# Optimization experiments

Hardware: AMD Instinct MI355X
Metric: run time of the kernel (lower is better)

The kernel has to match this reference:

```python
import jax, jax.numpy as jnp
import numpy as np

E = 32      # particle_embed_dim = q/k/v head out dim
G = 2       # nof_net_types (conv groups)
NEG_SLOPE = 0.01


def _glin(x, w, b, groups):
    """Grouped 1x1 conv on (M, C, 1, 1) == grouped linear.
    x: (M, Cin), w: (Cout, Cin//groups), b: (Cout,)."""
    M = x.shape[0]
    Cout = w.shape[0]
    xg = x.reshape(M, groups, -1)                 # (M, G, Cin/G)
    wg = w.reshape(groups, Cout // groups, -1)    # (G, Cout/G, Cin/G)
    y = jnp.einsum('mgi,goi->mgo', xg, wg).reshape(M, Cout)
    return y + b


def setup_inputs() -> dict:
    key = jax.random.key(0)
    ks = jax.random.split(key, 9)
    B, N = 32, 1024
    s = 0.05
    return {
        'x_e':   jax.random.normal(ks[0], (B, N, G * E), dtype=jnp.float32),
        'w_qkv': jax.random.normal(ks[1], (3 * G * E, E), dtype=jnp.float32) * s,
        'b_qkv': jax.random.normal(ks[2], (3 * G * E,), dtype=jnp.float32) * s,
        'w_h1':  jax.random.normal(ks[3], (G * E, 2 * E), dtype=jnp.float32) * s,
        'b_h1':  jax.random.normal(ks[4], (G * E,), dtype=jnp.float32) * s,
        'w_h10': jax.random.normal(ks[5], (G * E, E), dtype=jnp.float32) * s,
        'b_h10': jax.random.normal(ks[6], (G * E,), dtype=jnp.float32) * s,
        'w_h11': jax.random.normal(ks[7], (G * E, E), dtype=jnp.float32) * s,
        'b_h11': jax.random.normal(ks[8], (G * E,), dtype=jnp.float32) * s,
    }


def reference(x_e, w_qkv, b_qkv, w_h1, b_h1, w_h10, b_h10, w_h11, b_h11):
    B, N, D = x_e.shape                      # D = G*E = 64
    act = lambda z: jnp.where(z >= 0, z, NEG_SLOPE * z)

    # grouped 1x1-conv QKV projection
    qkv = _glin(x_e.reshape(B * N, D), w_qkv, b_qkv, G)        # (B*N, 3*G*E)
    qkv = qkv.reshape(B, N, G, 3, E).transpose(0, 2, 3, 1, 4)  # (B, G, 3, N, E)
    q, k, v = qkv[:, :, 0], qkv[:, :, 1], qkv[:, :, 2]         # each (B, G, N, E)

    # NOTE: module divides k by sqrt(E) and logits by sqrt(E) again -> 1/E total
    scale = 1.0 / E
    ip = jnp.einsum('bgne,bgme->bgnm', q, k) * scale           # (B, G, N, N)
    sip = jax.nn.softmax(ip, axis=-1)
    attn = jnp.einsum('bgnm,bgme->bgne', sip, v)               # (B, G, N, E)

    # concat pre-attention v with attention output, regroup per-particle
    x_xe = jnp.concatenate([v, attn], axis=3)                  # (B, G, N, 2E)
    x_xe = x_xe.transpose(0, 2, 1, 3).reshape(B * N, G * 2 * E)  # (B*N, 128)

    h = act(_glin(x_xe, w_h1, b_h1, G))
    h = act(_glin(h, w_h10, b_h10, G))
    h = act(_glin(h, w_h11, b_h11, G))
    return h.reshape(B * N, G * E, 1, 1)
```

## Files before the change

### kernel.cpp

```cpp
#include <hip/hip_runtime.h>

#define B_ 32
#define N_ 1024
#define NEG 0.01f
#define QSC (1.4426950408889634f/32.0f)

using half8  = __attribute__((ext_vector_type(8))) _Float16;
using half4  = __attribute__((ext_vector_type(4))) _Float16;
using half2  = __attribute__((ext_vector_type(2))) _Float16;
using fp16x2 = __attribute__((ext_vector_type(2))) __fp16;
using floatx4 = __attribute__((ext_vector_type(4))) float;

#if defined(__has_builtin)
#if __has_builtin(__builtin_amdgcn_exp2f)
#define EXP2(x) __builtin_amdgcn_exp2f(x)
#endif
#endif
#ifndef EXP2
#define EXP2(x) exp2f(x)
#endif

#define MFMA32 __builtin_amdgcn_mfma_f32_16x16x32_f16
#define MFMA16 __builtin_amdgcn_mfma_f32_16x16x16f16

__device__ inline half2 pkcvt(float a, float b) {
    fp16x2 r = __builtin_amdgcn_cvt_pkrtz(a, b);
    return __builtin_bit_cast(half2, r);
}

__device__ inline half8 cvt8(float4 a, float4 b) {
    half2 p0 = pkcvt(a.x, a.y);
    half2 p1 = pkcvt(a.z, a.w);
    half2 p2 = pkcvt(b.x, b.y);
    half2 p3 = pkcvt(b.z, b.w);
    half8 h = { p0[0],p0[1], p1[0],p1[1], p2[0],p2[1], p3[0],p3[1] };
    return h;
}

struct __align__(16) Smem {
    _Float16 wsh[96*36];
    float    bsh[96];
    _Float16 Kst[2][128*40];
    _Float16 Vtst[2][32*136];
    union {
        _Float16 qs[128*40];
        _Float16 xs[128*72];
    } u;
    float bl1[32], bl10[32], bl11[32];
};

__global__ __launch_bounds__(256, 2) void fused_kernel(
    const float* __restrict__ x, const float* __restrict__ w_qkv, const float* __restrict__ b_qkv,
    const float* __restrict__ w_h1,  const float* __restrict__ b_h1,
    const float* __restrict__ w_h10, const float* __restrict__ b_h10,
    const float* __restrict__ w_h11, const float* __restrict__ b_h11,
    float* __restrict__ out)
{
    __shared__ Smem sm;
    int t = threadIdx.x;
    int bid = blockIdx.x;
    int xcd = bid & 7, j = bid >> 3;
    int bg = xcd*8 + (j >> 3);
    int qtile = j & 7;
    int b = bg >> 1, g = bg & 1;
    int qbase = qtile * 128;
    int lane = t & 63, w = t >> 6;
    int L15 = lane & 15, quad = lane >> 4;

    for (int idx = t; idx < 96*32; idx += 256) {
        int r = idx >> 5, c = idx & 31;
        float wv = w_qkv[(g*96 + r)*32 + c];
        sm.wsh[r*36 + c] = (_Float16)(r < 32 ? wv*QSC : wv);
    }
    if (t < 96) sm.bsh[t] = b_qkv[g*96 + t];
    if (t < 32) {
        sm.bl1[t]  = b_h1[g*32+t];
        sm.bl10[t] = b_h10[g*32+t];
        sm.bl11[t] = b_h11[g*32+t];
    }
    __syncthreads();

    half8 bwq[2], bwk[2], bwv[2];
    floatx4 cq[2], ck[2], cv[2];
    #pragma unroll
    for (int et = 0; et < 2; et++) {
        bwq[et] = *(const half8*)&sm.wsh[(     et*16 + L15)*36 + quad*8];
        bwk[et] = *(const half8*)&sm.wsh[(32 + et*16 + L15)*36 + quad*8];
        bwv[et] = *(const half8*)&sm.wsh[(64 + et*16 + L15)*36 + quad*8];
        float bq = sm.bsh[     et*16 + L15] * QSC;
        float bk = sm.bsh[32 + et*16 + L15];
        float bv = sm.bsh[64 + et*16 + L15];
        cq[et] = (floatx4){bq,bq,bq,bq};
        ck[et] = (floatx4){bk,bk,bk,bk};
        cv[et] = (floatx4){bv,bv,bv,bv};
    }

    {
        floatx4 dq[2][2];
        #pragma unroll
        for (int mt = 0; mt < 2; mt++) {
            const float* p = x + ((size_t)b*N_ + qbase + w*32 + mt*16 + L15)*64 + g*32 + quad*8;
            half8 axq = cvt8(*(const float4*)p, *(const float4*)(p + 4));
            dq[mt][0] = MFMA32(axq, bwq[0], cq[0], 0,0,0);
            dq[mt][1] = MFMA32(axq, bwq[1], cq[1], 0,0,0);
        }
        #pragma unroll
        for (int mt = 0; mt < 2; mt++)
            #pragma unroll
            for (int et = 0; et < 2; et++)
                #pragma unroll
                for (int r = 0; r < 4; r++)
                    sm.u.qs[(w*32 + mt*16 + quad*4 + r)*40 + et*16 + L15] =
                        (_Float16)dq[mt][et][r];
    }
    __syncthreads();
    half8 bq0 = *(const half8*)&sm.u.qs[(w*32 +      L15)*40 + quad*8];
    half8 bq1 = *(const half8*)&sm.u.qs[(w*32 + 16 + L15)*40 + quad*8];
    __syncthreads();

    float4 xf0[2], xf1[2];
    auto prefetch = [&](int tile) {
        #pragma unroll
        for (int mt = 0; mt < 2; mt++) {
            const float* p = x + ((size_t)b*N_ + tile*128 + w*32 + mt*16 + L15)*64 + g*32 + quad*8;
            xf0[mt] = *(const float4*)p;
            xf1[mt] = *(const float4*)(p + 4);
        }
    };
    auto proj_tile = [&](int tile, int buf) {
        floatx4 dK[2][2], dV[2][2];
        #pragma unroll
        for (int mt = 0; mt < 2; mt++) {
            half8 axk = cvt8(xf0[mt], xf1[mt]);
            dK[mt][0] = MFMA32(axk, bwk[0], ck[0], 0,0,0);
            dK[mt][1] = MFMA32(axk, bwk[1], ck[1], 0,0,0);
            dV[mt][0] = MFMA32(axk, bwv[0], cv[0], 0,0,0);
            dV[mt][1] = MFMA32(axk, bwv[1], cv[1], 0,0,0);
        }
        #pragma unroll
        for (int mt = 0; mt < 2; mt++) {
            int rb = w*32 + mt*16 + quad*4;
            #pragma unroll
            for (int et = 0; et < 2; et++) {
                half2 k01 = pkcvt(dK[mt][et][0], dK[mt][et][1]);
                half2 k23 = pkcvt(dK[mt][et][2], dK[mt][et][3]);
                half2 v01 = pkcvt(dV[mt][et][0], dV[mt][et][1]);
                half2 v23 = pkcvt(dV[mt][et][2], dV[mt][et][3]);
                half4 vh = { v01[0], v01[1], v23[0], v23[1] };
                sm.Kst[buf][(rb+0)*40 + et*16 + L15] = k01[0];
                sm.Kst[buf][(rb+1)*40 + et*16 + L15] = k01[1];
                sm.Kst[buf][(rb+2)*40 + et*16 + L15] = k23[0];
                sm.Kst[buf][(rb+3)*40 + et*16 + L15] = k23[1];
                *(half4*)&sm.Vtst[buf][(et*16 + L15)*136 + rb] = vh;
                if (tile == qtile) {
                    #pragma unroll
                    for (int r = 0; r < 4; r++)
                        sm.u.xs[(rb + r)*72 + et*16 + L15] = vh[r];
                }
            }
        }
    };

    prefetch(0);
    proj_tile(0, 0);
    __syncthreads();

    floatx4 o00 = {0.f,0.f,0.f,0.f}, o01 = o00, o10 = o00, o11 = o00;
    float lsum0 = 0.f, lsum1 = 0.f;

    for (int kt = 0; kt < 8; kt++) {
        int cur = kt & 1;
        if (kt < 7) prefetch(kt + 1);
        __builtin_amdgcn_s_setprio(1);
        #pragma unroll
        for (int mt8 = 0; mt8 < 8; mt8++) {
            half8 ak = *(const half8*)&sm.Kst[cur][(mt8*16 + L15)*40 + quad*8];
            floatx4 zz = {0.f,0.f,0.f,0.f};
            floatx4 s0 = MFMA32(ak, bq0, zz, 0,0,0);
            floatx4 s1 = MFMA32(ak, bq1, zz, 0,0,0);
            float p00 = EXP2(s0.x), p01 = EXP2(s0.y), p02 = EXP2(s0.z), p03 = EXP2(s0.w);
            float p10 = EXP2(s1.x), p11 = EXP2(s1.y), p12 = EXP2(s1.z), p13 = EXP2(s1.w);
            lsum0 += (p00+p01)+(p02+p03);
            lsum1 += (p10+p11)+(p12+p13);
            half2 pa = pkcvt(p00, p01);
            half2 pb = pkcvt(p02, p03);
            half2 pc = pkcvt(p10, p11);
            half2 pd = pkcvt(p12, p13);
            half4 a0 = { pa[0], pa[1], pb[0], pb[1] };
            half4 a1 = { pc[0], pc[1], pd[0], pd[1] };
            half4 bv0 = *(const half4*)&sm.Vtst[cur][      L15*136 + mt8*16 + quad*4];
            half4 bv1 = *(const half4*)&sm.Vtst[cur][(16 + L15)*136 + mt8*16 + quad*4];
            o00 = MFMA16(a0, bv0, o00, 0,0,0);
            o01 = MFMA16(a0, bv1, o01, 0,0,0);
            o10 = MFMA16(a1, bv0, o10, 0,0,0);
            o11 = MFMA16(a1, bv1, o11, 0,0,0);
        }
        __builtin_amdgcn_s_setprio(0);
        if (kt < 7) {
            proj_tile(kt + 1, 1 - cur);
            __syncthreads();
        }
    }

    lsum0 += __shfl_xor(lsum0, 16, 64); lsum0 += __shfl_xor(lsum0, 32, 64);
    lsum1 += __shfl_xor(lsum1, 16, 64); lsum1 += __shfl_xor(lsum1, 32, 64);
    float inv0 = 1.0f / lsum0;
    float inv1 = 1.0f / lsum1;
    float li[2][4];
    #pragma unroll
    for (int r = 0; r < 4; r++) {
        li[0][r] = __shfl(inv0, quad*4 + r, 64);
        li[1][r] = __shfl(inv1, quad*4 + r, 64);
    }

    {
        const floatx4* ofr[2][2] = { {&o00,&o01}, {&o10,&o11} };
        #pragma unroll
        for (int nt = 0; nt < 2; nt++) {
            #pragma unroll
            for (int et = 0; et < 2; et++) {
                floatx4 ov = *ofr[nt][et];
                sm.u.xs[(w*32+nt*16+quad*4+0)*72 + 32 + et*16 + L15] = (_Float16)(ov[0]*li[nt][0]);
                sm.u.xs[(w*32+nt*16+quad*4+1)*72 + 32 + et*16 + L15] = (_Float16)(ov[1]*li[nt][1]);
                sm.u.xs[(w*32+nt*16+quad*4+2)*72 + 32 + et*16 + L15] = (_Float16)(ov[2]*li[nt][2]);
                sm.u.xs[(w*32+nt*16+quad*4+3)*72 + 32 + et*16 + L15] = (_Float16)(ov[3]*li[nt][3]);
            }
        }
    }

    half4 a1f[2][4], a2f[2][2], a3f[2][2];
    #pragma unroll
    for (int mt = 0; mt < 2; mt++) {
        #pragma unroll
        for (int kt = 0; kt < 4; kt++) {
            float4 f = *(const float4*)(w_h1 + (size_t)(g*32+mt*16+L15)*64 + kt*16 + quad*4);
            half2 ha = pkcvt(f.x, f.y);
            half2 hb = pkcvt(f.z, f.w);
            half4 h = { ha[0], ha[1], hb[0], hb[1] };
            a1f[mt][kt] = h;
        }
        #pragma unroll
        for (int kt = 0; kt < 2; kt++) {
            float4 f = *(const float4*)(w_h10 + (size_t)(g*32+mt*16+L15)*32 + kt*16 + quad*4);
            half2 ha = pkcvt(f.x, f.y);
            half2 hb = pkcvt(f.z, f.w);
            half4 h = { ha[0], ha[1], hb[0], hb[1] };
            a2f[mt][kt] = h;
            float4 f2 = *(const float4*)(w_h11 + (size_t)(g*32+mt*16+L15)*32 + kt*16 + quad*4);
            half2 hc = pkcvt(f2.x, f2.y);
            half2 hd = pkcvt(f2.z, f2.w);
            half4 h2 = { hc[0], hc[1], hd[0], hd[1] };
            a3f[mt][kt] = h2;
        }
    }

    floatx4 d1[2][2];
    #pragma unroll
    for (int mt = 0; mt < 2; mt++) {
        float4 bb = *(const float4*)&sm.bl1[mt*16 + quad*4];
        floatx4 seed = { bb.x, bb.y, bb.z, bb.w };
        d1[mt][0] = seed; d1[mt][1] = seed;
    }
    #pragma unroll
    for (int nt = 0; nt < 2; nt++)
        #pragma unroll
        for (int kt = 0; kt < 4; kt++) {
            half4 b1 = *(const half4*)&sm.u.xs[(w*32+nt*16+L15)*72 + kt*16 + quad*4];
            d1[0][nt] = MFMA16(a1f[0][kt], b1, d1[0][nt], 0,0,0);
            d1[1][nt] = MFMA16(a1f[1][kt], b1, d1[1][nt], 0,0,0);
        }
    half4 h1b[2][2];
    #pragma unroll
    for (int mt = 0; mt < 2; mt++)
        #pragma unroll
        for (int nt = 0; nt < 2; nt++) {
            float v0 = d1[mt][nt][0]; v0 = (v0>=0.f)?v0:NEG*v0;
            float v1 = d1[mt][nt][1]; v1 = (v1>=0.f)?v1:NEG*v1;
            float v2 = d1[mt][nt][2]; v2 = (v2>=0.f)?v2:NEG*v2;
            float v3 = d1[mt][nt][3]; v3 = (v3>=0.f)?v3:NEG*v3;
            half2 ha = pkcvt(v0, v1);
            half2 hb = pkcvt(v2, v3);
            half4 h = { ha[0], ha[1], hb[0], hb[1] };
            h1b[mt][nt] = h;
        }
    floatx4 d2[2][2];
    #pragma unroll
    for (int mt = 0; mt < 2; mt++) {
        float4 bb = *(const float4*)&sm.bl10[mt*16 + quad*4];
        floatx4 seed = { bb.x, bb.y, bb.z, bb.w };
        d2[mt][0] = seed; d2[mt][1] = seed;
    }
    #pragma unroll
    for (int mt = 0; mt < 2; mt++)
        #pragma unroll
        for (int nt = 0; nt < 2; nt++)
            #pragma unroll
            for (int kt = 0; kt < 2; kt++)
                d2[mt][nt] = MFMA16(a2f[mt][kt], h1b[kt][nt], d2[mt][nt], 0,0,0);
    half4 h2b[2][2];
    #pragma unroll
    for (int mt = 0; mt < 2; mt++)
        #pragma unroll
        for (int nt = 0; nt < 2; nt++) {
            float v0 = d2[mt][nt][0]; v0 = (v0>=0.f)?v0:NEG*v0;
            float v1 = d2[mt][nt][1]; v1 = (v1>=0.f)?v1:NEG*v1;
            float v2 = d2[mt][nt][2]; v2 = (v2>=0.f)?v2:NEG*v2;
            float v3 = d2[mt][nt][3]; v3 = (v3>=0.f)?v3:NEG*v3;
            half2 ha = pkcvt(v0, v1);
            half2 hb = pkcvt(v2, v3);
            half4 h = { ha[0], ha[1], hb[0], hb[1] };
            h2b[mt][nt] = h;
        }
    floatx4 d3[2][2];
    #pragma unroll
    for (int mt = 0; mt < 2; mt++) {
        float4 bb = *(const float4*)&sm.bl11[mt*16 + quad*4];
        floatx4 seed = { bb.x, bb.y, bb.z, bb.w };
        d3[mt][0] = seed; d3[mt][1] = seed;
    }
    #pragma unroll
    for (int mt = 0; mt < 2; mt++)
        #pragma unroll
        for (int nt = 0; nt < 2; nt++)
            #pragma unroll
            for (int kt = 0; kt < 2; kt++)
                d3[mt][nt] = MFMA16(a3f[mt][kt], h2b[kt][nt], d3[mt][nt], 0,0,0);
    #pragma unroll
    for (int mt = 0; mt < 2; mt++)
        #pragma unroll
        for (int nt = 0; nt < 2; nt++) {
            float4 ov;
            ov.x = d3[mt][nt][0]; ov.x = (ov.x>=0.f)?ov.x:NEG*ov.x;
            ov.y = d3[mt][nt][1]; ov.y = (ov.y>=0.f)?ov.y:NEG*ov.y;
            ov.z = d3[mt][nt][2]; ov.z = (ov.z>=0.f)?ov.z:NEG*ov.z;
            ov.w = d3[mt][nt][3]; ov.w = (ov.w>=0.f)?ov.w:NEG*ov.w;
            *(float4*)(out + ((size_t)b*N_ + qbase + w*32 + nt*16 + L15)*64 + g*32 + mt*16 + quad*4) = ov;
        }
}

extern "C" void kernel_launch(void* const* d_in, const int* in_sizes, int n_in,
                              void* d_out, int out_size, void* d_ws, size_t ws_size,
                              hipStream_t stream) {
    const float* x_e   = (const float*)d_in[0];
    const float* w_qkv = (const float*)d_in[1];
    const float* b_qkv = (const float*)d_in[2];
    const float* w_h1  = (const float*)d_in[3];
    const float* b_h1  = (const float*)d_in[4];
    const float* w_h10 = (const float*)d_in[5];
    const float* b_h10 = (const float*)d_in[6];
    const float* w_h11 = (const float*)d_in[7];
    const float* b_h11 = (const float*)d_in[8];
    float* out = (float*)d_out;

    hipLaunchKernelGGL(fused_kernel, dim3(B_*2*8), dim3(256), 0, stream,
                       x_e, w_qkv, b_qkv, w_h1, b_h1, w_h10, b_h10, w_h11, b_h11, out);
}
```

Measured before the change: 97.86 us.

## Share per-tile K/V projections across blocks via global workspace and flags

New measurement: 274.5 us. +180.5%, slower.

```diff
diff --git a/kernel.cpp b/kernel.cpp
--- a/kernel.cpp
+++ b/kernel.cpp
@@ -4,6 +4,7 @@
 #define N_ 1024
 #define NEG 0.01f
 #define QSC (1.4426950408889634f/32.0f)
+#define MAGIC 0x5EEDBEA7u
 
 using half8  = __attribute__((ext_vector_type(8))) _Float16;
 using half4  = __attribute__((ext_vector_type(4))) _Float16;
@@ -37,13 +38,18 @@
     return h;
 }
 
+__device__ __forceinline__ void gload16(const _Float16* g, _Float16* l) {
+    __builtin_amdgcn_global_load_lds(
+        (const __attribute__((address_space(1))) unsigned int*)g,
+        (__attribute__((address_space(3))) unsigned int*)l, 16, 0, 0);
+}
+
 struct __align__(16) Smem {
     _Float16 wsh[96*36];
     float    bsh[96];
-    _Float16 Kst[2][128*40];
-    _Float16 Vtst[2][32*136];
     union {
-        _Float16 qs[128*40];
+        struct { _Float16 qs[128*40]; _Float16 kst[128*32]; _Float16 vt[32*136]; } p1;
+        struct { _Float16 K[2][4096]; _Float16 Vt[2][4096]; } p2;
         _Float16 xs[128*72];
     } u;
     float bl1[32], bl10[32], bl11[32];
@@ -54,7 +60,8 @@
     const float* __restrict__ w_h1,  const float* __restrict__ b_h1,
     const float* __restrict__ w_h10, const float* __restrict__ b_h10,
     const float* __restrict__ w_h11, const float* __restrict__ b_h11,
-    float* __restrict__ out)
+    float* __restrict__ out, _Float16* __restrict__ Kg, _Float16* __restrict__ Vtg,
+    unsigned* __restrict__ flags)
 {
     __shared__ Smem sm;
     int t = threadIdx.x;
@@ -66,6 +73,7 @@
     int qbase = qtile * 128;
     int lane = t & 63, w = t >> 6;
     int L15 = lane & 15, quad = lane >> 4;
+    const floatx4 zz = {0.f,0.f,0.f,0.f};
 
     for (int idx = t; idx < 96*32; idx += 256) {
         int r = idx >> 5, c = idx & 31;
@@ -81,101 +89,114 @@
     __syncthreads();
 
     half8 bwq[2], bwk[2], bwv[2];
-    floatx4 cq[2], ck[2], cv[2];
+    float bqv[2], bvv[2];
     #pragma unroll
     for (int et = 0; et < 2; et++) {
         bwq[et] = *(const half8*)&sm.wsh[(     et*16 + L15)*36 + quad*8];
         bwk[et] = *(const half8*)&sm.wsh[(32 + et*16 + L15)*36 + quad*8];
         bwv[et] = *(const half8*)&sm.wsh[(64 + et*16 + L15)*36 + quad*8];
-        float bq = sm.bsh[     et*16 + L15] * QSC;
-        float bk = sm.bsh[32 + et*16 + L15];
-        float bv = sm.bsh[64 + et*16 + L15];
-        cq[et] = (floatx4){bq,bq,bq,bq};
-        ck[et] = (floatx4){bk,bk,bk,bk};
-        cv[et] = (floatx4){bv,bv,bv,bv};
-    }
+        bqv[et] = sm.bsh[     et*16 + L15] * QSC;
+        bvv[et] = sm.bsh[64 + et*16 + L15];
+    }
+
+    half4 vown[2][2];
+    #pragma unroll
+    for (int mt = 0; mt < 2; mt++) {
+        const float* p = x + ((size_t)b*N_ + qbase + w*32 + mt*16 + L15)*64 + g*32 + quad*8;
+        half8 ax = cvt8(*(const float4*)p, *(const float4*)(p + 4));
+        int rb = w*32 + mt*16 + quad*4;
+        #pragma unroll
+        for (int et = 0; et < 2; et++) {
+            floatx4 cq = {bqv[et],bqv[et],bqv[et],bqv[et]};
+            floatx4 cv = {bvv[et],bvv[et],bvv[et],bvv[et]};
+            floatx4 dq = MFMA32(ax, bwq[et], cq, 0,0,0);
+            floatx4 dk = MFMA32(ax, bwk[et], zz, 0,0,0);
+            floatx4 dv = MFMA32(ax, bwv[et], cv, 0,0,0);
+            #pragma unroll
+            for (int r = 0; r < 4; r++)
+                sm.u.p1.qs[(rb+r)*40 + et*16 + L15] = (_Float16)dq[r];
+            half2 k01 = pkcvt(dk[0], dk[1]);
+            half2 k23 = pkcvt(dk[2], dk[3]);
+            sm.u.p1.kst[(rb+0)*32 + et*16 + L15] = k01[0];
+            sm.u.p1.kst[(rb+1)*32 + et*16 + L15] = k01[1];
+            sm.u.p1.kst[(rb+2)*32 + et*16 + L15] = k23[0];
+            sm.u.p1.kst[(rb+3)*32 + et*16 + L15] = k23[1];
+            half2 v01 = pkcvt(dv[0], dv[1]);
+            half2 v23 = pkcvt(dv[2], dv[3]);
+            half4 vh = { v01[0], v01[1], v23[0], v23[1] };
+            *(half4*)&sm.u.p1.vt[(et*16 + L15)*136 + rb] = vh;
+            vown[mt][et] = vh;
+        }
+    }
+    __syncthreads();
+
+    half8 bq0 = *(const half8*)&sm.u.p1.qs[(w*32 +      L15)*40 + quad*8];
+    half8 bq1 = *(const half8*)&sm.u.p1.qs[(w*32 + 16 + L15)*40 + quad*8];
 
     {
-        floatx4 dq[2][2];
-        #pragma unroll
-        for (int mt = 0; mt < 2; mt++) {
-            const float* p = x + ((size_t)b*N_ + qbase + w*32 + mt*16 + L15)*64 + g*32 + quad*8;
-            half8 axq = cvt8(*(const float4*)p, *(const float4*)(p + 4));
-            dq[mt][0] = MFMA32(axq, bwq[0], cq[0], 0,0,0);
-            dq[mt][1] = MFMA32(axq, bwq[1], cq[1], 0,0,0);
-        }
-        #pragma unroll
-        for (int mt = 0; mt < 2; mt++)
-            #pragma unroll
-            for (int et = 0; et < 2; et++)
-                #pragma unroll
-                for (int r = 0; r < 4; r++)
-                    sm.u.qs[(w*32 + mt*16 + quad*4 + r)*40 + et*16 + L15] =
-                        (_Float16)dq[mt][et][r];
-    }
+        const float4* s4 = (const float4*)sm.u.p1.kst;
+        float4* d4 = (float4*)(Kg + (size_t)bg*32768 + (size_t)qbase*32);
+        d4[t] = s4[t];
+        d4[t+256] = s4[t+256];
+    }
+    {
+        int e = t >> 3, c = t & 7;
+        const float4* s4 = (const float4*)&sm.u.p1.vt[e*136 + c*16];
+        float4* d4 = (float4*)(Vtg + (size_t)bg*32768 + (size_t)e*1024 + qbase + c*16);
+        d4[0] = s4[0];
+        d4[1] = s4[1];
+    }
+
+    __threadfence();
     __syncthreads();
-    half8 bq0 = *(const half8*)&sm.u.qs[(w*32 +      L15)*40 + quad*8];
-    half8 bq1 = *(const half8*)&sm.u.qs[(w*32 + 16 + L15)*40 + quad*8];
+    if (t == 0)
+        __hip_atomic_store(&flags[bg*8 + qtile], MAGIC,
+                           __ATOMIC_RELEASE, __HIP_MEMORY_SCOPE_AGENT);
+
+    const _Float16* kgB = Kg  + (size_t)bg*32768;
+    const _Float16* vgB = Vtg + (size_t)bg*32768;
+    const unsigned* fB = &flags[bg*8];
+    auto wait_tile = [&](int tj) {
+        for (int s_ = 0; s_ < (1<<20); ++s_) {
+            if (__hip_atomic_load(&fB[tj], __ATOMIC_ACQUIRE,
+                                  __HIP_MEMORY_SCOPE_AGENT) == MAGIC)
+                break;
+        }
+    };
+    int kRow   = lane >> 2;
+    int kChunk = (lane & 3) ^ ((lane >> 3) & 3);
+
+    auto stage = [&](int tile, int bufi) {
+        #pragma unroll
+        for (int d = 0; d < 2; d++) {
+            gload16(kgB + (size_t)(tile*128 + w*32 + d*16 + kRow)*32 + kChunk*8,
+                    &sm.u.p2.K[bufi][w*1024 + d*512]);
+            int e  = w*8 + d*4 + (lane >> 4);
+            int vc = (lane & 15) ^ (e & 7);
+            gload16(vgB + (size_t)e*1024 + tile*128 + vc*8,
+                    &sm.u.p2.Vt[bufi][w*1024 + d*512]);
+        }
+    };
+
+    floatx4 o00 = zz, o01 = zz, o10 = zz, o11 = zz;
+    float lsum0 = 0.f, lsum1 = 0.f;
+    int kswz = (quad ^ ((L15 >> 1) & 3)) * 8;
+    int vswz = ((L15 & 7) << 1);
+
+    wait_tile(0);
+    stage(0, 0);
     __syncthreads();
-
-    float4 xf0[2], xf1[2];
-    auto prefetch = [&](int tile) {
-        #pragma unroll
-        for (int mt = 0; mt < 2; mt++) {
-            const float* p = x + ((size_t)b*N_ + tile*128 + w*32 + mt*16 + L15)*64 + g*32 + quad*8;
-            xf0[mt] = *(const float4*)p;
-            xf1[mt] = *(const float4*)(p + 4);
-        }
-    };
-    auto proj_tile = [&](int tile, int buf) {
-        floatx4 dK[2][2], dV[2][2];
-        #pragma unroll
-        for (int mt = 0; mt < 2; mt++) {
-            half8 axk = cvt8(xf0[mt], xf1[mt]);
-            dK[mt][0] = MFMA32(axk, bwk[0], ck[0], 0,0,0);
-            dK[mt][1] = MFMA32(axk, bwk[1], ck[1], 0,0,0);
-            dV[mt][0] = MFMA32(axk, bwv[0], cv[0], 0,0,0);
-            dV[mt][1] = MFMA32(axk, bwv[1], cv[1], 0,0,0);
-        }
-        #pragma unroll
-        for (int mt = 0; mt < 2; mt++) {
-            int rb = w*32 + mt*16 + quad*4;
-            #pragma unroll
-            for (int et = 0; et < 2; et++) {
-                half2 k01 = pkcvt(dK[mt][et][0], dK[mt][et][1]);
-                half2 k23 = pkcvt(dK[mt][et][2], dK[mt][et][3]);
-                half2 v01 = pkcvt(dV[mt][et][0], dV[mt][et][1]);
-                half2 v23 = pkcvt(dV[mt][et][2], dV[mt][et][3]);
-                half4 vh = { v01[0], v01[1], v23[0], v23[1] };
-                sm.Kst[buf][(rb+0)*40 + et*16 + L15] = k01[0];
-                sm.Kst[buf][(rb+1)*40 + et*16 + L15] = k01[1];
-                sm.Kst[buf][(rb+2)*40 + et*16 + L15] = k23[0];
-                sm.Kst[buf][(rb+3)*40 + et*16 + L15] = k23[1];
-                *(half4*)&sm.Vtst[buf][(et*16 + L15)*136 + rb] = vh;
-                if (tile == qtile) {
-                    #pragma unroll
-                    for (int r = 0; r < 4; r++)
-                        sm.u.xs[(rb + r)*72 + et*16 + L15] = vh[r];
-                }
-            }
-        }
-    };
-
-    prefetch(0);
-    proj_tile(0, 0);
-    __syncthreads();
-
-    floatx4 o00 = {0.f,0.f,0.f,0.f}, o01 = o00, o10 = o00, o11 = o00;
-    float lsum0 = 0.f, lsum1 = 0.f;
 
     for (int kt = 0; kt < 8; kt++) {
         int cur = kt & 1;
-        if (kt < 7) prefetch(kt + 1);
+        if (kt < 7) {
+            wait_tile(kt + 1);
+            stage(kt + 1, cur ^ 1);
+        }
         __builtin_amdgcn_s_setprio(1);
         #pragma unroll
-        for (int mt8 = 0; mt8 < 8; mt8++) {
-            half8 ak = *(const half8*)&sm.Kst[cur][(mt8*16 + L15)*40 + quad*8];
-            floatx4 zz = {0.f,0.f,0.f,0.f};
+        for (int m8 = 0; m8 < 8; m8++) {
+            half8 ak = *(const half8*)&sm.u.p2.K[cur][(m8*16 + L15)*32 + kswz];
             floatx4 s0 = MFMA32(ak, bq0, zz, 0,0,0);
             floatx4 s1 = MFMA32(ak, bq1, zz, 0,0,0);
             float p00 = EXP2(s0.x), p01 = EXP2(s0.y), p02 = EXP2(s0.z), p03 = EXP2(s0.w);
@@ -188,18 +209,16 @@
             half2 pd = pkcvt(p12, p13);
             half4 a0 = { pa[0], pa[1], pb[0], pb[1] };
             half4 a1 = { pc[0], pc[1], pd[0], pd[1] };
-            half4 bv0 = *(const half4*)&sm.Vtst[cur][      L15*136 + mt8*16 + quad*4];
-            half4 bv1 = *(const half4*)&sm.Vtst[cur][(16 + L15)*136 + mt8*16 + quad*4];
+            int vg_ = ((m8*4 + quad) ^ vswz) * 4;
+            half4 bv0 = *(const half4*)&sm.u.p2.Vt[cur][      L15*128 + vg_];
+            half4 bv1 = *(const half4*)&sm.u.p2.Vt[cur][(16 + L15)*128 + vg_];
             o00 = MFMA16(a0, bv0, o00, 0,0,0);
             o01 = MFMA16(a0, bv1, o01, 0,0,0);
             o10 = MFMA16(a1, bv0, o10, 0,0,0);
             o11 = MFMA16(a1, bv1, o11, 0,0,0);
         }
         __builtin_amdgcn_s_setprio(0);
-        if (kt < 7) {
-            proj_tile(kt + 1, 1 - cur);
-            __syncthreads();
-        }
+        __syncthreads();
     }
 
     lsum0 += __shfl_xor(lsum0, 16, 64); lsum0 += __shfl_xor(lsum0, 32, 64);
@@ -217,13 +236,17 @@
         const floatx4* ofr[2][2] = { {&o00,&o01}, {&o10,&o11} };
         #pragma unroll
         for (int nt = 0; nt < 2; nt++) {
+            int rb = w*32 + nt*16 + quad*4;
             #pragma unroll
             for (int et = 0; et < 2; et++) {
+                #pragma unroll
+                for (int r = 0; r < 4; r++)
+                    sm.u.xs[(rb+r)*72 + et*16 + L15] = vown[nt][et][r];
                 floatx4 ov = *ofr[nt][et];
-                sm.u.xs[(w*32+nt*16+quad*4+0)*72 + 32 + et*16 + L15] = (_Float16)(ov[0]*li[nt][0]);
-                sm.u.xs[(w*32+nt*16+quad*4+1)*72 + 32 + et*16 + L15] = (_Float16)(ov[1]*li[nt][1]);
-                sm.u.xs[(w*32+nt*16+quad*4+2)*72 + 32 + et*16 + L15] = (_Float16)(ov[2]*li[nt][2]);
-                sm.u.xs[(w*32+nt*16+quad*4+3)*72 + 32 + et*16 + L15] = (_Float16)(ov[3]*li[nt][3]);
+                sm.u.xs[(rb+0)*72 + 32 + et*16 + L15] = (_Float16)(ov[0]*li[nt][0]);
+                sm.u.xs[(rb+1)*72 + 32 + et*16 + L15] = (_Float16)(ov[1]*li[nt][1]);
+                sm.u.xs[(rb+2)*72 + 32 + et*16 + L15] = (_Float16)(ov[2]*li[nt][2]);
+                sm.u.xs[(rb+3)*72 + 32 + et*16 + L15] = (_Float16)(ov[3]*li[nt][3]);
             }
         }
     }
@@ -352,6 +375,11 @@
     const float* b_h11 = (const float*)d_in[8];
     float* out = (float*)d_out;
 
-    hipLaunchKernelGGL(fused_kernel, dim3(B_*2*8), dim3(256), 0, stream,
-                       x_e, w_qkv, b_qkv, w_h1, b_h1, w_h10, b_h10, w_h11, b_h11, out);
-}
+    _Float16* Kg   = (_Float16*)d_ws;
+    _Float16* Vtg  = (_Float16*)d_ws + (1u<<21);
+    unsigned* flags = (unsigned*)((_Float16*)d_ws + (2u<<21));
+
+    hipLaunchKernelGGL(fused_kernel, dim3(512), dim3(256), 0, stream,
+                       x_e, w_qkv, b_qkv, w_h1, b_h1, w_h10, b_h10, w_h11, b_h11,
+                       out, Kg, Vtg, flags);
+}
```

## Shrink shared memory and registers to raise occupancy to three blocks per CU

Applied to the files above, without the earlier changes.

Result: slower. 111.1 us (+13.5%).

```diff
diff --git a/kernel.cpp b/kernel.cpp
--- a/kernel.cpp
+++ b/kernel.cpp
@@ -40,16 +40,17 @@
 struct __align__(16) Smem {
     _Float16 wsh[96*36];
     float    bsh[96];
-    _Float16 Kst[2][128*40];
-    _Float16 Vtst[2][32*136];
     union {
-        _Float16 qs[128*40];
+        struct {
+            _Float16 Kst[2][128*36];
+            _Float16 Vtst[2][32*136];
+        } a;
         _Float16 xs[128*72];
     } u;
     float bl1[32], bl10[32], bl11[32];
 };
 
-__global__ __launch_bounds__(256, 2) void fused_kernel(
+__global__ __launch_bounds__(256, 3) void fused_kernel(
     const float* __restrict__ x, const float* __restrict__ w_qkv, const float* __restrict__ b_qkv,
     const float* __restrict__ w_h1,  const float* __restrict__ b_h1,
     const float* __restrict__ w_h10, const float* __restrict__ b_h10,
@@ -66,6 +67,7 @@
     int qbase = qtile * 128;
     int lane = t & 63, w = t >> 6;
     int L15 = lane & 15, quad = lane >> 4;
+    const floatx4 zz = {0.f,0.f,0.f,0.f};
 
     for (int idx = t; idx < 96*32; idx += 256) {
         int r = idx >> 5, c = idx & 31;
@@ -81,43 +83,37 @@
     __syncthreads();
 
     half8 bwq[2], bwk[2], bwv[2];
-    floatx4 cq[2], ck[2], cv[2];
+    floatx4 cv[2];
     #pragma unroll
     for (int et = 0; et < 2; et++) {
         bwq[et] = *(const half8*)&sm.wsh[(     et*16 + L15)*36 + quad*8];
         bwk[et] = *(const half8*)&sm.wsh[(32 + et*16 + L15)*36 + quad*8];
         bwv[et] = *(const half8*)&sm.wsh[(64 + et*16 + L15)*36 + quad*8];
-        float bq = sm.bsh[     et*16 + L15] * QSC;
-        float bk = sm.bsh[32 + et*16 + L15];
         float bv = sm.bsh[64 + et*16 + L15];
-        cq[et] = (floatx4){bq,bq,bq,bq};
-        ck[et] = (floatx4){bk,bk,bk,bk};
         cv[et] = (floatx4){bv,bv,bv,bv};
     }
 
-    {
-        floatx4 dq[2][2];
-        #pragma unroll
-        for (int mt = 0; mt < 2; mt++) {
-            const float* p = x + ((size_t)b*N_ + qbase + w*32 + mt*16 + L15)*64 + g*32 + quad*8;
-            half8 axq = cvt8(*(const float4*)p, *(const float4*)(p + 4));
-            dq[mt][0] = MFMA32(axq, bwq[0], cq[0], 0,0,0);
-            dq[mt][1] = MFMA32(axq, bwq[1], cq[1], 0,0,0);
-        }
-        #pragma unroll
-        for (int mt = 0; mt < 2; mt++)
-            #pragma unroll
-            for (int et = 0; et < 2; et++)
-                #pragma unroll
-                for (int r = 0; r < 4; r++)
-                    sm.u.qs[(w*32 + mt*16 + quad*4 + r)*40 + et*16 + L15] =
-                        (_Float16)dq[mt][et][r];
+    _Float16* qs = sm.u.a.Kst[1];
+
+    #pragma unroll
+    for (int mt = 0; mt < 2; mt++) {
+        const float* p = x + ((size_t)b*N_ + qbase + w*32 + mt*16 + L15)*64 + g*32 + quad*8;
+        half8 axq = cvt8(*(const float4*)p, *(const float4*)(p + 4));
+        #pragma unroll
+        for (int et = 0; et < 2; et++) {
+            float bq = sm.bsh[et*16 + L15] * QSC;
+            floatx4 cq = {bq,bq,bq,bq};
+            floatx4 dq = MFMA32(axq, bwq[et], cq, 0,0,0);
+            #pragma unroll
+            for (int r = 0; r < 4; r++)
+                qs[(w*32 + mt*16 + quad*4 + r)*36 + et*16 + L15] = (_Float16)dq[r];
+        }
     }
     __syncthreads();
-    half8 bq0 = *(const half8*)&sm.u.qs[(w*32 +      L15)*40 + quad*8];
-    half8 bq1 = *(const half8*)&sm.u.qs[(w*32 + 16 + L15)*40 + quad*8];
-    __syncthreads();
-
+    half8 bq0 = *(const half8*)&qs[(w*32 +      L15)*36 + quad*8];
+    half8 bq1 = *(const half8*)&qs[(w*32 + 16 + L15)*36 + quad*8];
+
+    half4 vown[2][2];
     float4 xf0[2], xf1[2];
     auto prefetch = [&](int tile) {
         #pragma unroll
@@ -132,8 +128,8 @@
         #pragma unroll
         for (int mt = 0; mt < 2; mt++) {
             half8 axk = cvt8(xf0[mt], xf1[mt]);
-            dK[mt][0] = MFMA32(axk, bwk[0], ck[0], 0,0,0);
-            dK[mt][1] = MFMA32(axk, bwk[1], ck[1], 0,0,0);
+            dK[mt][0] = MFMA32(axk, bwk[0], zz, 0,0,0);
+            dK[mt][1] = MFMA32(axk, bwk[1], zz, 0,0,0);
             dV[mt][0] = MFMA32(axk, bwv[0], cv[0], 0,0,0);
             dV[mt][1] = MFMA32(axk, bwv[1], cv[1], 0,0,0);
         }
@@ -147,16 +143,12 @@
                 half2 v01 = pkcvt(dV[mt][et][0], dV[mt][et][1]);
                 half2 v23 = pkcvt(dV[mt][et][2], dV[mt][et][3]);
                 half4 vh = { v01[0], v01[1], v23[0], v23[1] };
-                sm.Kst[buf][(rb+0)*40 + et*16 + L15] = k01[0];
-                sm.Kst[buf][(rb+1)*40 + et*16 + L15] = k01[1];
-                sm.Kst[buf][(rb+2)*40 + et*16 + L15] = k23[0];
-                sm.Kst[buf][(rb+3)*40 + et*16 + L15] = k23[1];
-                *(half4*)&sm.Vtst[buf][(et*16 + L15)*136 + rb] = vh;
-                if (tile == qtile) {
-                    #pragma unroll
-                    for (int r = 0; r < 4; r++)
-                        sm.u.xs[(rb + r)*72 + et*16 + L15] = vh[r];
-                }
+                sm.u.a.Kst[buf][(rb+0)*36 + et*16 + L15] = k01[0];
+                sm.u.a.Kst[buf][(rb+1)*36 + et*16 + L15] = k01[1];
+                sm.u.a.Kst[buf][(rb+2)*36 + et*16 + L15] = k23[0];
+                sm.u.a.Kst[buf][(rb+3)*36 + et*16 + L15] = k23[1];
+                *(half4*)&sm.u.a.Vtst[buf][(et*16 + L15)*136 + rb] = vh;
+                if (tile == qtile) vown[mt][et] = vh;
             }
         }
     };
@@ -165,7 +157,7 @@
     proj_tile(0, 0);
     __syncthreads();
 
-    floatx4 o00 = {0.f,0.f,0.f,0.f}, o01 = o00, o10 = o00, o11 = o00;
+    floatx4 o00 = zz, o01 = zz, o10 = zz, o11 = zz;
     float lsum0 = 0.f, lsum1 = 0.f;
 
     for (int kt = 0; kt < 8; kt++) {
@@ -173,9 +165,8 @@
         if (kt < 7) prefetch(kt + 1);
         __builtin_amdgcn_s_setprio(1);
         #pragma unroll
-        for (int mt8 = 0; mt8 < 8; mt8++) {
-            half8 ak = *(const half8*)&sm.Kst[cur][(mt8*16 + L15)*40 + quad*8];
-            floatx4 zz = {0.f,0.f,0.f,0.f};
+        for (int m8 = 0; m8 < 8; m8++) {
+            half8 ak = *(const half8*)&sm.u.a.Kst[cur][(m8*16 + L15)*36 + quad*8];
             floatx4 s0 = MFMA32(ak, bq0, zz, 0,0,0);
             floatx4 s1 = MFMA32(ak, bq1, zz, 0,0,0);
             float p00 = EXP2(s0.x), p01 = EXP2(s0.y), p02 = EXP2(s0.z), p03 = EXP2(s0.w);
@@ -188,8 +179,8 @@
             half2 pd = pkcvt(p12, p13);
             half4 a0 = { pa[0], pa[1], pb[0], pb[1] };
             half4 a1 = { pc[0], pc[1], pd[0], pd[1] };
-            half4 bv0 = *(const half4*)&sm.Vtst[cur][      L15*136 + mt8*16 + quad*4];
-            half4 bv1 = *(const half4*)&sm.Vtst[cur][(16 + L15)*136 + mt8*16 + quad*4];
+            half4 bv0 = *(const half4*)&sm.u.a.Vtst[cur][      L15*136 + m8*16 + quad*4];
+            half4 bv1 = *(const half4*)&sm.u.a.Vtst[cur][(16 + L15)*136 + m8*16 + quad*4];
             o00 = MFMA16(a0, bv0, o00, 0,0,0);
             o01 = MFMA16(a0, bv1, o01, 0,0,0);
             o10 = MFMA16(a1, bv0, o10, 0,0,0);
@@ -201,6 +192,7 @@
             __syncthreads();
         }
     }
+    __syncthreads();
 
     lsum0 += __shfl_xor(lsum0, 16, 64); lsum0 += __shfl_xor(lsum0, 32, 64);
     lsum1 += __shfl_xor(lsum1, 16, 64); lsum1 += __shfl_xor(lsum1, 32, 64);
@@ -217,13 +209,17 @@
         const floatx4* ofr[2][2] = { {&o00,&o01}, {&o10,&o11} };
         #pragma unroll
         for (int nt = 0; nt < 2; nt++) {
+            int rb = w*32 + nt*16 + quad*4;
             #pragma unroll
             for (int et = 0; et < 2; et++) {
+                #pragma unroll
+                for (int r = 0; r < 4; r++)
+                    sm.u.xs[(rb+r)*72 + et*16 + L15] = vown[nt][et][r];
                 floatx4 ov = *ofr[nt][et];
-                sm.u.xs[(w*32+nt*16+quad*4+0)*72 + 32 + et*16 + L15] = (_Float16)(ov[0]*li[nt][0]);
-                sm.u.xs[(w*32+nt*16+quad*4+1)*72 + 32 + et*16 + L15] = (_Float16)(ov[1]*li[nt][1]);
-                sm.u.xs[(w*32+nt*16+quad*4+2)*72 + 32 + et*16 + L15] = (_Float16)(ov[2]*li[nt][2]);
-                sm.u.xs[(w*32+nt*16+quad*4+3)*72 + 32 + et*16 + L15] = (_Float16)(ov[3]*li[nt][3]);
+                sm.u.xs[(rb+0)*72 + 32 + et*16 + L15] = (_Float16)(ov[0]*li[nt][0]);
+                sm.u.xs[(rb+1)*72 + 32 + et*16 + L15] = (_Float16)(ov[1]*li[nt][1]);
+                sm.u.xs[(rb+2)*72 + 32 + et*16 + L15] = (_Float16)(ov[2]*li[nt][2]);
+                sm.u.xs[(rb+3)*72 + 32 + et*16 + L15] = (_Float16)(ov[3]*li[nt][3]);
             }
         }
     }
```
